# Kernel tuning notes

Measured on AMD Instinct MI355X. Metric: run time of the kernel, lower is better.

Reference implementation:

```python
import jax, jax.numpy as jnp
import numpy as np

M, N, F = 8192, 4096, 1


def quat_to_rotmat(q):
    # q: [N,4] (w,x,y,z) -> [N,3,3]
    q = q / jnp.linalg.norm(q, axis=-1, keepdims=True)
    w, x, y, z = q[:, 0], q[:, 1], q[:, 2], q[:, 3]
    r00 = 1 - 2 * (y * y + z * z)
    r01 = 2 * (x * y - w * z)
    r02 = 2 * (x * z + w * y)
    r10 = 2 * (x * y + w * z)
    r11 = 1 - 2 * (x * x + z * z)
    r12 = 2 * (y * z - w * x)
    r20 = 2 * (x * z - w * y)
    r21 = 2 * (y * z + w * x)
    r22 = 1 - 2 * (x * x + y * y)
    R = jnp.stack([jnp.stack([r00, r01, r02], -1),
                   jnp.stack([r10, r11, r12], -1),
                   jnp.stack([r20, r21, r22], -1)], -2)
    return R


def setup_inputs() -> dict:
    key = jax.random.key(0)
    k1, k2, k3, k4, k5, k6 = jax.random.split(key, 6)
    points = jax.random.normal(k1, (M, 3), dtype=jnp.float32)
    xyz = jax.random.normal(k2, (N, 3), dtype=jnp.float32)
    scale_raw = jax.random.normal(k3, (N, 3), dtype=jnp.float32) * 0.5  # _scale param
    rotation_raw = jax.random.normal(k4, (N, 4), dtype=jnp.float32)     # _rotation param
    opacity_raw = jax.random.normal(k5, (N, 1), dtype=jnp.float32)      # _opacity param
    features = jax.random.normal(k6, (N, F), dtype=jnp.float32)         # _features param
    return {"points": points, "xyz": xyz, "scale_raw": scale_raw,
            "rotation_raw": rotation_raw, "opacity_raw": opacity_raw,
            "features": features}


def reference(points, xyz, scale_raw, rotation_raw, opacity_raw, features):
    scale = jnp.exp(scale_raw)                       # [N,3] activation
    R = quat_to_rotmat(rotation_raw)                 # [N,3,3]
    RS = R * scale[:, None, :]                       # R @ diag(scale)
    cov = jnp.einsum('nik,njk->nij', RS, RS)         # [N,3,3]
    cov_inv = jnp.linalg.inv(cov)                    # [N,3,3]
    diff = points[:, None, :] - xyz[None, :, :]      # [M,N,3]
    mahal = jnp.einsum('mni,nij,mnj->mn', diff, cov_inv, diff)  # [M,N]
    influence = jnp.exp(-0.5 * mahal)                # [M,N]
    opacity = jax.nn.sigmoid(opacity_raw)            # [N,1]
    weights = influence * opacity.T                  # [M,N]
    values = weights @ features                      # [M,F]
    return values, weights
```

## Files before the change

kernel.cpp:

```cpp
#include <hip/hip_runtime.h>


#define THREADS 256
#define N_PER_THREAD 4
#define N_PER_BLOCK (THREADS * N_PER_THREAD)
#define M_PER_BLOCK 16

__global__ void gauss_precomp(const float* __restrict__ xyz,
                              const float* __restrict__ scale_raw,
                              const float* __restrict__ rot_raw,
                              const float* __restrict__ op_raw,
                              const float* __restrict__ feat,
                              float4* __restrict__ P, int N) {
  int n = blockIdx.x * blockDim.x + threadIdx.x;
  if (n >= N) return;
  float qw = rot_raw[4*n+0], qx = rot_raw[4*n+1], qy = rot_raw[4*n+2], qz = rot_raw[4*n+3];
  float inorm = rsqrtf(qw*qw + qx*qx + qy*qy + qz*qz);
  qw *= inorm; qx *= inorm; qy *= inorm; qz *= inorm;
  float sx = expf(scale_raw[3*n+0]);
  float sy = expf(scale_raw[3*n+1]);
  float sz = expf(scale_raw[3*n+2]);
  float r00 = 1.f - 2.f*(qy*qy + qz*qz);
  float r01 = 2.f*(qx*qy - qw*qz);
  float r02 = 2.f*(qx*qz + qw*qy);
  float r10 = 2.f*(qx*qy + qw*qz);
  float r11 = 1.f - 2.f*(qx*qx + qz*qz);
  float r12 = 2.f*(qy*qz - qw*qx);
  float r20 = 2.f*(qx*qz - qw*qy);
  float r21 = 2.f*(qy*qz + qw*qx);
  float r22 = 1.f - 2.f*(qx*qx + qy*qy);
  float a0 = r00*sx, a1 = r01*sy, a2 = r02*sz;
  float b0 = r10*sx, b1 = r11*sy, b2 = r12*sz;
  float c0 = r20*sx, c1 = r21*sy, c2 = r22*sz;
  float c00 = a0*a0 + a1*a1 + a2*a2;
  float c01 = a0*b0 + a1*b1 + a2*b2;
  float c02 = a0*c0 + a1*c1 + a2*c2;
  float c11 = b0*b0 + b1*b1 + b2*b2;
  float c12 = b0*c0 + b1*c1 + b2*c2;
  float c22 = c0*c0 + c1*c1 + c2*c2;
  float m00 = c11*c22 - c12*c12;
  float m01 = c02*c12 - c01*c22;
  float m02 = c01*c12 - c02*c11;
  float det = c00*m00 + c01*m01 + c02*m02;
  float idet = 1.f / det;
  float i00 = m00*idet;
  float i01 = m01*idet;
  float i02 = m02*idet;
  float i11 = (c00*c22 - c02*c02)*idet;
  float i12 = (c02*c01 - c00*c12)*idet;
  float i22 = (c00*c11 - c01*c01)*idet;
  float op = 1.f / (1.f + expf(-op_raw[n]));
  float f  = feat[n];
  P[n*3+0] = make_float4(xyz[3*n+0], xyz[3*n+1], xyz[3*n+2], op);
  P[n*3+1] = make_float4(i00, i01, i02, i11);
  P[n*3+2] = make_float4(i12, i22, f, 0.f);
}

__global__ __launch_bounds__(THREADS) void gauss_sweep(
    const float* __restrict__ points,
    const float4* __restrict__ P,
    float* __restrict__ weights,
    float* __restrict__ partials,
    int M, int N) {
  const int t = threadIdx.x;
  const int n0 = blockIdx.x * N_PER_BLOCK + t * N_PER_THREAD;
  const int mbase = blockIdx.y * M_PER_BLOCK;

  float4 ga[N_PER_THREAD], gb[N_PER_THREAD], gc[N_PER_THREAD];
#pragma unroll
  for (int j = 0; j < N_PER_THREAD; ++j) {
    int n = n0 + j;
    ga[j] = P[n*3+0];
    gb[j] = P[n*3+1];
    gc[j] = P[n*3+2];
  }

  const int wave = t >> 6;
  const int pidx = blockIdx.x * 4 + wave;

#pragma unroll 4
  for (int i = 0; i < M_PER_BLOCK; ++i) {
    const int m = mbase + i;
    const float px = points[3*m+0];
    const float py = points[3*m+1];
    const float pz = points[3*m+2];

    float4 w;
    float vsum = 0.f;
#pragma unroll
    for (int j = 0; j < N_PER_THREAD; ++j) {
      const float dx = px - ga[j].x;
      const float dy = py - ga[j].y;
      const float dz = pz - ga[j].z;
      const float t0 = gb[j].x*dx + gb[j].y*dy + gb[j].z*dz;
      const float t1 = gb[j].y*dx + gb[j].w*dy + gc[j].x*dz;
      const float t2 = gb[j].z*dx + gc[j].x*dy + gc[j].y*dz;
      const float mahal = dx*t0 + dy*t1 + dz*t2;
      const float wj = __expf(-0.5f * mahal) * ga[j].w;
      (&w.x)[j] = wj;
      vsum += wj * gc[j].z;
    }
    *(float4*)&weights[(size_t)m * N + n0] = w;

#pragma unroll
    for (int off = 32; off >= 1; off >>= 1)
      vsum += __shfl_xor(vsum, off, 64);
    if ((t & 63) == 0)
      partials[(size_t)m * 16 + pidx] = vsum;
  }
}

__global__ void gauss_finalize(const float* __restrict__ partials,
                               float* __restrict__ values, int M) {
  int m = blockIdx.x * blockDim.x + threadIdx.x;
  if (m >= M) return;
  const float4* p = (const float4*)&partials[(size_t)m * 16];
  float4 a = p[0], b = p[1], c = p[2], d = p[3];
  values[m] = ((a.x + a.y) + (a.z + a.w)) + ((b.x + b.y) + (b.z + b.w)) +
              ((c.x + c.y) + (c.z + c.w)) + ((d.x + d.y) + (d.z + d.w));
}

extern "C" void kernel_launch(void* const* d_in, const int* in_sizes, int n_in,
                              void* d_out, int out_size, void* d_ws, size_t ws_size,
                              hipStream_t stream) {
  const float* points   = (const float*)d_in[0];
  const float* xyz      = (const float*)d_in[1];
  const float* scale_raw= (const float*)d_in[2];
  const float* rot_raw  = (const float*)d_in[3];
  const float* op_raw   = (const float*)d_in[4];
  const float* feat     = (const float*)d_in[5];

  const int M = in_sizes[0] / 3;
  const int N = in_sizes[1] / 3;
  const int F = in_sizes[5] / N;
  (void)F;

  float* values  = (float*)d_out;
  float* weights = (float*)d_out + (size_t)M;

  float4* P       = (float4*)d_ws;
  float* partials = (float*)((char*)d_ws + (size_t)N * 48);

  gauss_precomp<<<(N + THREADS - 1) / THREADS, THREADS, 0, stream>>>(
      xyz, scale_raw, rot_raw, op_raw, feat, P, N);

  dim3 grid(N / N_PER_BLOCK, M / M_PER_BLOCK);
  gauss_sweep<<<grid, THREADS, 0, stream>>>(points, P, weights, partials, M, N);

  gauss_finalize<<<(M + THREADS - 1) / THREADS, THREADS, 0, stream>>>(
      partials, values, M);
}
```

Baseline: 40.30 us.

## Fuse precompute, sweep and reduction into one kernel covering all gaussians per block

Merges the three launches into one. Each block handles 16 points across all 4096 gaussians, and each thread recomputes the inverse covariance for its 16 gaussians in registers. The per-point reduction finishes in shared memory, so the partials buffer and the finalize kernel go away. Opacity is folded into the exponent as a log2 term so each weight costs one exp2 plus an FMA. This saves two launches and the workspace round-trip, but every block redoes the gaussian preprocessing and register pressure rises, with the sizes now hardcoded.

```diff
diff --git a/kernel.cpp b/kernel.cpp
--- a/kernel.cpp
+++ b/kernel.cpp
@@ -2,151 +2,155 @@
 
 
 #define THREADS 256
-#define N_PER_THREAD 4
-#define N_PER_BLOCK (THREADS * N_PER_THREAD)
-#define M_PER_BLOCK 16
+#define JPT 4
+#define CHUNKS 4
+#define MPB 16
+#define NN 4096
+#define MM 8192
 
-__global__ void gauss_precomp(const float* __restrict__ xyz,
-                              const float* __restrict__ scale_raw,
-                              const float* __restrict__ rot_raw,
-                              const float* __restrict__ op_raw,
-                              const float* __restrict__ feat,
-                              float4* __restrict__ P, int N) {
-  int n = blockIdx.x * blockDim.x + threadIdx.x;
-  if (n >= N) return;
-  float qw = rot_raw[4*n+0], qx = rot_raw[4*n+1], qy = rot_raw[4*n+2], qz = rot_raw[4*n+3];
-  float inorm = rsqrtf(qw*qw + qx*qx + qy*qy + qz*qz);
-  qw *= inorm; qx *= inorm; qy *= inorm; qz *= inorm;
-  float sx = expf(scale_raw[3*n+0]);
-  float sy = expf(scale_raw[3*n+1]);
-  float sz = expf(scale_raw[3*n+2]);
-  float r00 = 1.f - 2.f*(qy*qy + qz*qz);
-  float r01 = 2.f*(qx*qy - qw*qz);
-  float r02 = 2.f*(qx*qz + qw*qy);
-  float r10 = 2.f*(qx*qy + qw*qz);
-  float r11 = 1.f - 2.f*(qx*qx + qz*qz);
-  float r12 = 2.f*(qy*qz - qw*qx);
-  float r20 = 2.f*(qx*qz - qw*qy);
-  float r21 = 2.f*(qy*qz + qw*qx);
-  float r22 = 1.f - 2.f*(qx*qx + qy*qy);
-  float a0 = r00*sx, a1 = r01*sy, a2 = r02*sz;
-  float b0 = r10*sx, b1 = r11*sy, b2 = r12*sz;
-  float c0 = r20*sx, c1 = r21*sy, c2 = r22*sz;
-  float c00 = a0*a0 + a1*a1 + a2*a2;
-  float c01 = a0*b0 + a1*b1 + a2*b2;
-  float c02 = a0*c0 + a1*c1 + a2*c2;
-  float c11 = b0*b0 + b1*b1 + b2*b2;
-  float c12 = b0*c0 + b1*c1 + b2*c2;
-  float c22 = c0*c0 + c1*c1 + c2*c2;
-  float m00 = c11*c22 - c12*c12;
-  float m01 = c02*c12 - c01*c22;
-  float m02 = c01*c12 - c02*c11;
-  float det = c00*m00 + c01*m01 + c02*m02;
-  float idet = 1.f / det;
-  float i00 = m00*idet;
-  float i01 = m01*idet;
-  float i02 = m02*idet;
-  float i11 = (c00*c22 - c02*c02)*idet;
-  float i12 = (c02*c01 - c00*c12)*idet;
-  float i22 = (c00*c11 - c01*c01)*idet;
-  float op = 1.f / (1.f + expf(-op_raw[n]));
-  float f  = feat[n];
-  P[n*3+0] = make_float4(xyz[3*n+0], xyz[3*n+1], xyz[3*n+2], op);
-  P[n*3+1] = make_float4(i00, i01, i02, i11);
-  P[n*3+2] = make_float4(i12, i22, f, 0.f);
-}
+__global__ __launch_bounds__(THREADS, 2) void gauss_fused(
+    const float* __restrict__ points,
+    const float* __restrict__ xyz,
+    const float* __restrict__ scale_raw,
+    const float* __restrict__ rot_raw,
+    const float* __restrict__ op_raw,
+    const float* __restrict__ feat,
+    float* __restrict__ values,
+    float* __restrict__ weights) {
+  const int t = threadIdx.x;
+  const int mbase = blockIdx.x * MPB;
 
-__global__ __launch_bounds__(THREADS) void gauss_sweep(
-    const float* __restrict__ points,
-    const float4* __restrict__ P,
-    float* __restrict__ weights,
-    float* __restrict__ partials,
-    int M, int N) {
-  const int t = threadIdx.x;
-  const int n0 = blockIdx.x * N_PER_BLOCK + t * N_PER_THREAD;
-  const int mbase = blockIdx.y * M_PER_BLOCK;
+  float gx[CHUNKS][JPT], gy[CHUNKS][JPT], gz[CHUNKS][JPT];
+  float i00[CHUNKS][JPT], i01[CHUNKS][JPT], i02[CHUNKS][JPT];
+  float i11[CHUNKS][JPT], i12[CHUNKS][JPT], i22[CHUNKS][JPT];
+  float lop[CHUNKS][JPT], gf[CHUNKS][JPT];
 
-  float4 ga[N_PER_THREAD], gb[N_PER_THREAD], gc[N_PER_THREAD];
 #pragma unroll
-  for (int j = 0; j < N_PER_THREAD; ++j) {
-    int n = n0 + j;
-    ga[j] = P[n*3+0];
-    gb[j] = P[n*3+1];
-    gc[j] = P[n*3+2];
+  for (int c = 0; c < CHUNKS; ++c) {
+    const int nb = c * (NN / CHUNKS) + t * JPT;
+    const float4* rot4 = (const float4*)(rot_raw + 4 * (size_t)nb);
+    const float4 q0 = rot4[0], q1 = rot4[1], q2 = rot4[2], q3 = rot4[3];
+    const float4* sc4 = (const float4*)(scale_raw + 3 * (size_t)nb);
+    const float4 s0 = sc4[0], s1 = sc4[1], s2 = sc4[2];
+    const float4* xy4 = (const float4*)(xyz + 3 * (size_t)nb);
+    const float4 p0 = xy4[0], p1 = xy4[1], p2 = xy4[2];
+    const float4 op4 = *(const float4*)(op_raw + nb);
+    const float4 f4  = *(const float4*)(feat + nb);
+
+    const float4 q[JPT] = {q0, q1, q2, q3};
+    const float sxa[JPT] = {s0.x, s0.w, s1.z, s2.y};
+    const float sya[JPT] = {s0.y, s1.x, s1.w, s2.z};
+    const float sza[JPT] = {s0.z, s1.y, s2.x, s2.w};
+    const float xxa[JPT] = {p0.x, p0.w, p1.z, p2.y};
+    const float yya[JPT] = {p0.y, p1.x, p1.w, p2.z};
+    const float zza[JPT] = {p0.z, p1.y, p2.x, p2.w};
+    const float opa[JPT] = {op4.x, op4.y, op4.z, op4.w};
+    const float fa[JPT]  = {f4.x, f4.y, f4.z, f4.w};
+
+#pragma unroll
+    for (int j = 0; j < JPT; ++j) {
+      float qw = q[j].x, qx = q[j].y, qy = q[j].z, qz = q[j].w;
+      const float inorm = rsqrtf(qw*qw + qx*qx + qy*qy + qz*qz);
+      qw *= inorm; qx *= inorm; qy *= inorm; qz *= inorm;
+      const float sx = __expf(sxa[j]);
+      const float sy = __expf(sya[j]);
+      const float sz = __expf(sza[j]);
+      const float r00 = 1.f - 2.f*(qy*qy + qz*qz);
+      const float r01 = 2.f*(qx*qy - qw*qz);
+      const float r02 = 2.f*(qx*qz + qw*qy);
+      const float r10 = 2.f*(qx*qy + qw*qz);
+      const float r11 = 1.f - 2.f*(qx*qx + qz*qz);
+      const float r12 = 2.f*(qy*qz - qw*qx);
+      const float r20 = 2.f*(qx*qz - qw*qy);
+      const float r21 = 2.f*(qy*qz + qw*qx);
+      const float r22 = 1.f - 2.f*(qx*qx + qy*qy);
+      const float a0 = r00*sx, a1 = r01*sy, a2 = r02*sz;
+      const float b0 = r10*sx, b1 = r11*sy, b2 = r12*sz;
+      const float c0 = r20*sx, c1 = r21*sy, c2 = r22*sz;
+      const float c00 = a0*a0 + a1*a1 + a2*a2;
+      const float c01 = a0*b0 + a1*b1 + a2*b2;
+      const float c02 = a0*c0 + a1*c1 + a2*c2;
+      const float c11 = b0*b0 + b1*b1 + b2*b2;
+      const float c12 = b0*c0 + b1*c1 + b2*c2;
+      const float c22 = c0*c0 + c1*c1 + c2*c2;
+      const float m00 = c11*c22 - c12*c12;
+      const float m01 = c02*c12 - c01*c22;
+      const float m02 = c01*c12 - c02*c11;
+      const float det = c00*m00 + c01*m01 + c02*m02;
+      const float idet = 1.f / det;
+      i00[c][j] = m00*idet;
+      i01[c][j] = m01*idet;
+      i02[c][j] = m02*idet;
+      i11[c][j] = (c00*c22 - c02*c02)*idet;
+      i12[c][j] = (c02*c01 - c00*c12)*idet;
+      i22[c][j] = (c00*c11 - c01*c01)*idet;
+      gx[c][j] = xxa[j]; gy[c][j] = yya[j]; gz[c][j] = zza[j];
+      lop[c][j] = -__log2f(1.f + __expf(-opa[j]));
+      gf[c][j] = fa[j];
+    }
   }
 
-  const int wave = t >> 6;
-  const int pidx = blockIdx.x * 4 + wave;
+  float vs[MPB];
+  const int wv = t >> 6;
+  __shared__ float part[MPB][THREADS / 64];
 
-#pragma unroll 4
-  for (int i = 0; i < M_PER_BLOCK; ++i) {
+#pragma unroll 2
+  for (int i = 0; i < MPB; ++i) {
     const int m = mbase + i;
     const float px = points[3*m+0];
     const float py = points[3*m+1];
     const float pz = points[3*m+2];
-
-    float4 w;
     float vsum = 0.f;
 #pragma unroll
-    for (int j = 0; j < N_PER_THREAD; ++j) {
-      const float dx = px - ga[j].x;
-      const float dy = py - ga[j].y;
-      const float dz = pz - ga[j].z;
-      const float t0 = gb[j].x*dx + gb[j].y*dy + gb[j].z*dz;
-      const float t1 = gb[j].y*dx + gb[j].w*dy + gc[j].x*dz;
-      const float t2 = gb[j].z*dx + gc[j].x*dy + gc[j].y*dz;
-      const float mahal = dx*t0 + dy*t1 + dz*t2;
-      const float wj = __expf(-0.5f * mahal) * ga[j].w;
-      (&w.x)[j] = wj;
-      vsum += wj * gc[j].z;
+    for (int c = 0; c < CHUNKS; ++c) {
+      float4 w;
+#pragma unroll
+      for (int j = 0; j < JPT; ++j) {
+        const float dx = px - gx[c][j];
+        const float dy = py - gy[c][j];
+        const float dz = pz - gz[c][j];
+        const float t0 = i00[c][j]*dx + i01[c][j]*dy + i02[c][j]*dz;
+        const float t1 = i01[c][j]*dx + i11[c][j]*dy + i12[c][j]*dz;
+        const float t2 = i02[c][j]*dx + i12[c][j]*dy + i22[c][j]*dz;
+        const float mahal = dx*t0 + dy*t1 + dz*t2;
+        const float wj = exp2f(fmaf(mahal, -0.72134752044448170f, lop[c][j]));
+        (&w.x)[j] = wj;
+        vsum = fmaf(wj, gf[c][j], vsum);
+      }
+      *(float4*)&weights[(size_t)m * NN + c * (NN / CHUNKS) + t * JPT] = w;
     }
-    *(float4*)&weights[(size_t)m * N + n0] = w;
+    vs[i] = vsum;
+  }
 
 #pragma unroll
+  for (int i = 0; i < MPB; ++i) {
+#pragma unroll
     for (int off = 32; off >= 1; off >>= 1)
-      vsum += __shfl_xor(vsum, off, 64);
-    if ((t & 63) == 0)
-      partials[(size_t)m * 16 + pidx] = vsum;
+      vs[i] += __shfl_xor(vs[i], off, 64);
   }
-}
-
-__global__ void gauss_finalize(const float* __restrict__ partials,
-                               float* __restrict__ values, int M) {
-  int m = blockIdx.x * blockDim.x + threadIdx.x;
-  if (m >= M) return;
-  const float4* p = (const float4*)&partials[(size_t)m * 16];
-  float4 a = p[0], b = p[1], c = p[2], d = p[3];
-  values[m] = ((a.x + a.y) + (a.z + a.w)) + ((b.x + b.y) + (b.z + b.w)) +
-              ((c.x + c.y) + (c.z + c.w)) + ((d.x + d.y) + (d.z + d.w));
+  if ((t & 63) == 0) {
+#pragma unroll
+    for (int i = 0; i < MPB; ++i) part[i][wv] = vs[i];
+  }
+  __syncthreads();
+  if (t < MPB) {
+    values[mbase + t] = (part[t][0] + part[t][1]) + (part[t][2] + part[t][3]);
+  }
 }
 
 extern "C" void kernel_launch(void* const* d_in, const int* in_sizes, int n_in,
                               void* d_out, int out_size, void* d_ws, size_t ws_size,
                               hipStream_t stream) {
-  const float* points   = (const float*)d_in[0];
-  const float* xyz      = (const float*)d_in[1];
-  const float* scale_raw= (const float*)d_in[2];
-  const float* rot_raw  = (const float*)d_in[3];
-  const float* op_raw   = (const float*)d_in[4];
-  const float* feat     = (const float*)d_in[5];
-
-  const int M = in_sizes[0] / 3;
-  const int N = in_sizes[1] / 3;
-  const int F = in_sizes[5] / N;
-  (void)F;
+  const float* points    = (const float*)d_in[0];
+  const float* xyz       = (const float*)d_in[1];
+  const float* scale_raw = (const float*)d_in[2];
+  const float* rot_raw   = (const float*)d_in[3];
+  const float* op_raw    = (const float*)d_in[4];
+  const float* feat      = (const float*)d_in[5];
 
   float* values  = (float*)d_out;
-  float* weights = (float*)d_out + (size_t)M;
+  float* weights = (float*)d_out + MM;
 
-  float4* P       = (float4*)d_ws;
-  float* partials = (float*)((char*)d_ws + (size_t)N * 48);
-
-  gauss_precomp<<<(N + THREADS - 1) / THREADS, THREADS, 0, stream>>>(
-      xyz, scale_raw, rot_raw, op_raw, feat, P, N);
-
-  dim3 grid(N / N_PER_BLOCK, M / M_PER_BLOCK);
-  gauss_sweep<<<grid, THREADS, 0, stream>>>(points, P, weights, partials, M, N);
-
-  gauss_finalize<<<(M + THREADS - 1) / THREADS, THREADS, 0, stream>>>(
-      partials, values, M);
+  gauss_fused<<<MM / MPB, THREADS, 0, stream>>>(
+      points, xyz, scale_raw, rot_raw, op_raw, feat, values, weights);
 }
```

After: 38.74 us. -3.9%, faster.
